# Kernel optimization log

Hardware: AMD Instinct MI355X
Metric: run time of the kernel (lower is better)

## Reference

```python
import jax, jax.numpy as jnp
import numpy as np

B, Q, E, NH, L, P = 8, 1024, 256, 8, 4, 4
DH = E // NH
SHAPES = np.array([[128, 128], [64, 64], [32, 32], [16, 16]], dtype=np.int64)
STARTS = np.concatenate([[0], np.cumsum(SHAPES.prod(1))[:-1]]).astype(np.int64)
S_TOTAL = int(SHAPES.prod(1).sum())
EPS = 1e-5


def setup_inputs() -> dict:
    key = jax.random.key(0)
    ks = iter(jax.random.split(key, 40))
    def rn(shp, s=0.02):
        return jax.random.normal(next(ks), shp, jnp.float32) * s
    return {
        "tgt": rn((B, Q, E), 1.0),
        "query_pos": rn((B, Q, E), 1.0),
        "reference_points": jax.random.uniform(next(ks), (B, Q, L, 2), jnp.float32),
        "src": rn((B, S_TOTAL, E), 1.0),
        "spatial_shapes": jnp.asarray(SHAPES),
        "level_start_index": jnp.asarray(STARTS),
        "in_proj_w": rn((3 * E, E)), "in_proj_b": jnp.zeros((3 * E,), jnp.float32),
        "out_proj_w": rn((E, E)), "out_proj_b": jnp.zeros((E,), jnp.float32),
        "norm1_g": jnp.ones((E,), jnp.float32), "norm1_b": jnp.zeros((E,), jnp.float32),
        "off_w": rn((NH * L * P * 2, E)), "off_b": rn((NH * L * P * 2,), 0.5),
        "aw_w": rn((NH * L * P, E)), "aw_b": jnp.zeros((NH * L * P,), jnp.float32),
        "vp_w": rn((E, E)), "vp_b": jnp.zeros((E,), jnp.float32),
        "op_w": rn((E, E)), "op_b": jnp.zeros((E,), jnp.float32),
        "norm2_g": jnp.ones((E,), jnp.float32), "norm2_b": jnp.zeros((E,), jnp.float32),
        "w1": rn((4 * E, E)), "b1": jnp.zeros((4 * E,), jnp.float32),
        "w2": rn((E, 4 * E)), "b2": jnp.zeros((E,), jnp.float32),
        "norm3_g": jnp.ones((E,), jnp.float32), "norm3_b": jnp.zeros((E,), jnp.float32),
    }


def _ln(x, g, b):
    mu = x.mean(-1, keepdims=True)
    var = ((x - mu) ** 2).mean(-1, keepdims=True)
    return (x - mu) * jax.lax.rsqrt(var + EPS) * g + b


def _bilinear(v, loc, Hl, Wl):
    # v: [B,NH,S_l,DH], loc in [0,1]: [B,NH,Q,P,2] -> [B,NH,Q,P,DH]
    # matches torch grid_sample(align_corners=False, padding='zeros')
    x = loc[..., 0] * Wl - 0.5
    y = loc[..., 1] * Hl - 0.5
    x0 = jnp.floor(x)
    y0 = jnp.floor(y)
    wx = (x - x0)[..., None]
    wy = (y - y0)[..., None]
    def g(yi, xi):
        valid = ((xi >= 0) & (xi <= Wl - 1) & (yi >= 0) & (yi <= Hl - 1)).astype(v.dtype)
        idx = (jnp.clip(yi, 0, Hl - 1) * Wl + jnp.clip(xi, 0, Wl - 1)).astype(jnp.int32)
        out = jnp.take_along_axis(v, idx.reshape(B, NH, Q * P, 1), axis=2)
        return out.reshape(B, NH, Q, P, DH) * valid[..., None]
    v00 = g(y0, x0); v01 = g(y0, x0 + 1.0)
    v10 = g(y0 + 1.0, x0); v11 = g(y0 + 1.0, x0 + 1.0)
    return (v00 * (1 - wy) * (1 - wx) + v01 * (1 - wy) * wx
            + v10 * wy * (1 - wx) + v11 * wy * wx)


def _forward(tgt, query_pos, reference_points, src,
             in_proj_w, in_proj_b, out_proj_w, out_proj_b, norm1_g, norm1_b,
             off_w, off_b, aw_w, aw_b, vp_w, vp_b, op_w, op_b,
             norm2_g, norm2_b, w1, b1, w2, b2, norm3_g, norm3_b,
             spatial_shapes, level_start_index):
    shp = np.asarray(spatial_shapes)
    starts = np.asarray(level_start_index)
    # ---- self-attention (q = k = tgt + pos, v = tgt) ----
    qk = tgt + query_pos
    wq, wk, wv = jnp.split(in_proj_w, 3, axis=0)
    bq, bk, bv = jnp.split(in_proj_b, 3, axis=0)
    q = (qk @ wq.T + bq).reshape(B, Q, NH, DH)
    k = (qk @ wk.T + bk).reshape(B, Q, NH, DH)
    v = (tgt @ wv.T + bv).reshape(B, Q, NH, DH)
    scores = jnp.einsum("bqhd,bkhd->bhqk", q, k) / jnp.sqrt(jnp.float32(DH))
    attn = jax.nn.softmax(scores, axis=-1)
    ctx = jnp.einsum("bhqk,bkhd->bqhd", attn, v).reshape(B, Q, E)
    tgt = _ln(tgt + (ctx @ out_proj_w.T + out_proj_b), norm1_g, norm1_b)
    # ---- MSDA cross-attention ----
    query = tgt + query_pos
    value = (src @ vp_w.T + vp_b).reshape(B, S_TOTAL, NH, DH).transpose(0, 2, 1, 3)  # [B,NH,S,DH]
    off = (query @ off_w.T + off_b).reshape(B, Q, NH, L, P, 2)
    aw = jax.nn.softmax((query @ aw_w.T + aw_b).reshape(B, Q, NH, L * P), -1)
    aw = aw.reshape(B, Q, NH, L, P)
    normalizer = jnp.asarray(shp[:, ::-1].copy(), jnp.float32)  # [L,2] = (W,H)
    loc = reference_points[:, :, None, :, None, :] + off / normalizer[None, None, None, :, None, :]
    loc = jnp.transpose(loc, (0, 2, 1, 3, 4, 5))  # [B,NH,Q,L,P,2]
    awt = jnp.transpose(aw, (0, 2, 1, 3, 4))      # [B,NH,Q,L,P]
    out = jnp.zeros((B, NH, Q, DH), jnp.float32)
    for l in range(L):
        Hl, Wl = int(shp[l, 0]), int(shp[l, 1])
        s0 = int(starts[l])
        vl = value[:, :, s0:s0 + Hl * Wl]
        samp = _bilinear(vl, loc[:, :, :, l], Hl, Wl)         # [B,NH,Q,P,DH]
        out = out + (samp * awt[:, :, :, l, :, None]).sum(3)
    ca = out.transpose(0, 2, 1, 3).reshape(B, Q, E) @ op_w.T + op_b
    tgt = _ln(tgt + ca, norm2_g, norm2_b)
    # ---- FFN ----
    h = jax.nn.relu(tgt @ w1.T + b1) @ w2.T + b2
    return _ln(tgt + h, norm3_g, norm3_b)


def reference(tgt, query_pos, reference_points, src, spatial_shapes, level_start_index,
              in_proj_w, in_proj_b, out_proj_w, out_proj_b, norm1_g, norm1_b,
              off_w, off_b, aw_w, aw_b, vp_w, vp_b, op_w, op_b,
              norm2_g, norm2_b, w1, b1, w2, b2, norm3_g, norm3_b):
    return _forward(tgt, query_pos, reference_points, src,
                    in_proj_w, in_proj_b, out_proj_w, out_proj_b, norm1_g, norm1_b,
                    off_w, off_b, aw_w, aw_b, vp_w, vp_b, op_w, op_b,
                    norm2_g, norm2_b, w1, b1, w2, b2, norm3_g, norm3_b,
                    spatial_shapes, level_start_index)
```

## Files before the change

### kernel.cpp

```cpp
#include <hip/hip_runtime.h>
#include <hip/hip_bf16.h>
#include <math.h>

typedef __hip_bfloat16 bf16;
typedef unsigned short ushort_t;

#define BQ 8
#define QLEN 1024
#define EMB 256
#define NHD 8
#define NLVL 4
#define NPT 4
#define DHD 32
#define STOT 21760

typedef short s8v __attribute__((ext_vector_type(8)));
typedef float f4v __attribute__((ext_vector_type(4)));

__device__ __forceinline__ float b2f(bf16 x) { return __bfloat162float(x); }

__device__ __forceinline__ float ldin(const void* p, int bf, size_t i) {
    return bf ? __bfloat162float(((const bf16*)p)[i]) : ((const float*)p)[i];
}

__device__ __forceinline__ float bfraw(unsigned u) {
    union { unsigned i; float f; } c; c.i = u << 16; return c.f;
}

__device__ __forceinline__ unsigned short f2us(float x) {
    bf16 h = __float2bfloat16(x);
    unsigned short u;
    __builtin_memcpy(&u, &h, 2);
    return u;
}

__global__ void detect_dtype(const unsigned* __restrict__ n1g, int* __restrict__ flag) {
    if (threadIdx.x == 0) flag[0] = (n1g[0] == 0x3F800000u) ? 0 : 1;
}

template <bool ARAW, bool RELU, typename CT, int WR, int WC>
__global__ __launch_bounds__(64 * WR * WC) void gemm_mfma(
        const void* __restrict__ A,
        const void* __restrict__ W, int w0,
        const void* __restrict__ bias, int b0,
        CT* __restrict__ C,
        int M, int N, int K,
        const int* __restrict__ dflag) {
    constexpr int T = 64 * WR * WC;
    constexpr int BM = 64 * WR, BN = 64 * WC;
    constexpr int AI = (BM * 4) / T;
    constexpr int BI = (BN * 4) / T;
    const int bfm = *dflag;
    __shared__ ushort_t As[BM][40];
    __shared__ ushort_t Bs[BN][40];
    const int tid = threadIdx.x;
    const int lane = tid & 63;
    const int wv = tid >> 6;
    const int wrow = (wv % WR) << 6;
    const int wcol = (wv / WR) << 6;
    const int m0 = blockIdx.x * BM, n0 = blockIdx.y * BN;
    const int l15 = lane & 15, lhi = lane >> 4;

    f4v acc[4][4] = {};

    uint4 ra[AI], rb[BI];
    float4 fa[AI][2], fb[BI][2];

    auto ld = [&](int k0) {
#pragma unroll
        for (int i = 0; i < AI; ++i) {
            const int idx = tid + T * i;
            const int r = idx >> 2, c = (idx & 3) << 3;
            const size_t aoff = (size_t)(m0 + r) * K + k0 + c;
            if (!ARAW || bfm) {
                ra[i] = *(const uint4*)((const ushort_t*)A + aoff);
            } else {
                const float* af = (const float*)A + aoff;
                fa[i][0] = *(const float4*)af;
                fa[i][1] = *(const float4*)(af + 4);
            }
        }
#pragma unroll
        for (int i = 0; i < BI; ++i) {
            const int idx = tid + T * i;
            const int r = idx >> 2, c = (idx & 3) << 3;
            const size_t woff = (size_t)(w0 + n0 + r) * K + k0 + c;
            if (bfm) {
                rb[i] = *(const uint4*)((const ushort_t*)W + woff);
            } else {
                const float* wf = (const float*)W + woff;
                fb[i][0] = *(const float4*)wf;
                fb[i][1] = *(const float4*)(wf + 4);
            }
        }
    };
    auto st = [&]() {
#pragma unroll
        for (int i = 0; i < AI; ++i) {
            const int idx = tid + T * i;
            const int r = idx >> 2, c = (idx & 3) << 3;
            if (!ARAW || bfm) {
                *(uint4*)&As[r][c] = ra[i];
            } else {
                ushort_t t[8] = {f2us(fa[i][0].x), f2us(fa[i][0].y), f2us(fa[i][0].z), f2us(fa[i][0].w),
                                 f2us(fa[i][1].x), f2us(fa[i][1].y), f2us(fa[i][1].z), f2us(fa[i][1].w)};
                *(uint4*)&As[r][c] = *(uint4*)t;
            }
        }
#pragma unroll
        for (int i = 0; i < BI; ++i) {
            const int idx = tid + T * i;
            const int r = idx >> 2, c = (idx & 3) << 3;
            if (bfm) {
                *(uint4*)&Bs[r][c] = rb[i];
            } else {
                ushort_t t[8] = {f2us(fb[i][0].x), f2us(fb[i][0].y), f2us(fb[i][0].z), f2us(fb[i][0].w),
                                 f2us(fb[i][1].x), f2us(fb[i][1].y), f2us(fb[i][1].z), f2us(fb[i][1].w)};
                *(uint4*)&Bs[r][c] = *(uint4*)t;
            }
        }
    };

    ld(0);
    for (int k0 = 0; k0 < K; k0 += 32) {
        st();
        __syncthreads();
        if (k0 + 32 < K) ld(k0 + 32);

        s8v afr[4], bfr[4];
#pragma unroll
        for (int i = 0; i < 4; ++i)
            afr[i] = *(const s8v*)&As[wrow + i * 16 + l15][lhi * 8];
#pragma unroll
        for (int j = 0; j < 4; ++j)
            bfr[j] = *(const s8v*)&Bs[wcol + j * 16 + l15][lhi * 8];
#pragma unroll
        for (int i = 0; i < 4; ++i)
#pragma unroll
            for (int j = 0; j < 4; ++j)
                acc[i][j] = __builtin_amdgcn_mfma_f32_16x16x32_bf16(
                    afr[i], bfr[j], acc[i][j], 0, 0, 0);
        __syncthreads();
    }

#pragma unroll
    for (int j = 0; j < 4; ++j) {
        const int n = n0 + wcol + j * 16 + l15;
        const float bv = ldin(bias, bfm, b0 + n);
#pragma unroll
        for (int i = 0; i < 4; ++i) {
#pragma unroll
            for (int p = 0; p < 4; ++p) {
                const int m = m0 + wrow + i * 16 + lhi * 4 + p;
                float v = acc[i][j][p] + bv;
                if (RELU) v = fmaxf(v, 0.f);
                if (sizeof(CT) == 2) ((ushort_t*)C)[(size_t)m * N + n] = f2us(v);
                else                 ((float*)C)[(size_t)m * N + n] = v;
            }
        }
    }
}

__global__ void ew_add_bf(const void* __restrict__ a, const void* __restrict__ b,
                          ushort_t* __restrict__ c, int n, const int* __restrict__ dflag) {
    const int bfm = *dflag;
    int i = blockIdx.x * 256 + threadIdx.x;
    if (i < n) c[i] = f2us(ldin(a, bfm, i) + ldin(b, bfm, i));
}

__global__ __launch_bounds__(256) void attn_mfma(const ushort_t* __restrict__ qkbuf,
                                                 const ushort_t* __restrict__ v,
                                                 ushort_t* __restrict__ ctx) {
    __shared__ ushort_t Ks[64][40];
    __shared__ ushort_t Vt[32][72];
    __shared__ ushort_t Ps[4][16][72];
    const int bh = blockIdx.y;
    const int b = bh >> 3, h = bh & 7;
    const int qt = blockIdx.x;
    const int tid = threadIdx.x;
    const int lane = tid & 63;
    const int wv = tid >> 6;
    const int l15 = lane & 15, quad = lane >> 4;
    const float scale = 0.17677669529663689f;

    const int qbase = (qt << 6) + (wv << 4);
    const s8v qfrag = *(const s8v*)(qkbuf +
        ((size_t)(b * QLEN + qbase + l15)) * 512 + h * DHD + quad * 8);

    const int sk = tid >> 2;
    const int sd = (tid & 3) << 3;

    float m_run[4] = {-1e30f, -1e30f, -1e30f, -1e30f};
    float l_run[4] = {};
    f4v o[2] = {};

    for (int kt = 0; kt < 16; ++kt) {
        __syncthreads();
        const size_t krow = (size_t)(b * QLEN + (kt << 6) + sk);
        *(uint4*)&Ks[sk][sd] = *(const uint4*)(qkbuf + krow * 512 + 256 + h * DHD + sd);
        const uint4 uv = *(const uint4*)(v + krow * 256 + h * DHD + sd);
        ushort_t vt[8];
        *(uint4*)vt = uv;
#pragma unroll
        for (int j = 0; j < 8; ++j) Vt[sd + j][sk] = vt[j];
        __syncthreads();

        f4v s4[4];
#pragma unroll
        for (int kb = 0; kb < 4; ++kb) {
            const s8v kfr = *(const s8v*)&Ks[(kb << 4) + l15][quad * 8];
            s4[kb] = __builtin_amdgcn_mfma_f32_16x16x32_bf16(qfrag, kfr, f4v{}, 0, 0, 0);
        }

        float sc[4][4];
#pragma unroll
        for (int kb = 0; kb < 4; ++kb)
#pragma unroll
            for (int p = 0; p < 4; ++p) sc[kb][p] = s4[kb][p] * scale;
        float mp[4];
#pragma unroll
        for (int p = 0; p < 4; ++p)
            mp[p] = fmaxf(fmaxf(sc[0][p], sc[1][p]), fmaxf(sc[2][p], sc[3][p]));
#pragma unroll
        for (int p = 0; p < 4; ++p) {
            mp[p] = fmaxf(mp[p], __shfl_xor(mp[p], 1, 64));
            mp[p] = fmaxf(mp[p], __shfl_xor(mp[p], 2, 64));
            mp[p] = fmaxf(mp[p], __shfl_xor(mp[p], 4, 64));
            mp[p] = fmaxf(mp[p], __shfl_xor(mp[p], 8, 64));
        }
        float al[4], ls[4] = {};
#pragma unroll
        for (int p = 0; p < 4; ++p) {
            const float mn = fmaxf(m_run[p], mp[p]);
            al[p] = __expf(m_run[p] - mn);
            m_run[p] = mn;
        }
        float pe[4][4];
#pragma unroll
        for (int kb = 0; kb < 4; ++kb)
#pragma unroll
            for (int p = 0; p < 4; ++p) {
                const float e = __expf(sc[kb][p] - m_run[p]);
                pe[kb][p] = e;
                ls[p] += e;
            }
#pragma unroll
        for (int p = 0; p < 4; ++p) {
            ls[p] += __shfl_xor(ls[p], 1, 64);
            ls[p] += __shfl_xor(ls[p], 2, 64);
            ls[p] += __shfl_xor(ls[p], 4, 64);
            ls[p] += __shfl_xor(ls[p], 8, 64);
            l_run[p] = l_run[p] * al[p] + ls[p];
        }
#pragma unroll
        for (int nb = 0; nb < 2; ++nb)
#pragma unroll
            for (int p = 0; p < 4; ++p) o[nb][p] *= al[p];

#pragma unroll
        for (int kb = 0; kb < 4; ++kb)
#pragma unroll
            for (int p = 0; p < 4; ++p)
                Ps[wv][(quad << 2) + p][(kb << 4) + l15] = f2us(pe[kb][p]);

#pragma unroll
        for (int kk = 0; kk < 2; ++kk) {
            const s8v afr = *(const s8v*)&Ps[wv][l15][kk * 32 + quad * 8];
#pragma unroll
            for (int nb = 0; nb < 2; ++nb) {
                const s8v bfr = *(const s8v*)&Vt[nb * 16 + l15][kk * 32 + quad * 8];
                o[nb] = __builtin_amdgcn_mfma_f32_16x16x32_bf16(afr, bfr, o[nb], 0, 0, 0);
            }
        }
    }

#pragma unroll
    for (int p = 0; p < 4; ++p) {
        const float inv = 1.f / l_run[p];
        const size_t row = (size_t)(b * QLEN + qbase + (quad << 2) + p) * EMB + h * DHD;
#pragma unroll
        for (int nb = 0; nb < 2; ++nb)
            ctx[row + nb * 16 + l15] = f2us(o[nb][p] * inv);
    }
}

__global__ __launch_bounds__(256) void ln_kernel(const void* __restrict__ xb,
                                                 const float* __restrict__ xf1,
                                                 const float* __restrict__ xf2,
                                                 const void* __restrict__ g,
                                                 const void* __restrict__ bta,
                                                 float* __restrict__ out_f,
                                                 ushort_t* __restrict__ out_b,
                                                 void* __restrict__ out_d,
                                                 const void* __restrict__ qp,
                                                 ushort_t* __restrict__ out_q,
                                                 const int* __restrict__ dflag) {
    const int bf = *dflag;
    const int row = blockIdx.x, t = threadIdx.x;
    const size_t base = (size_t)row * EMB + t;
    float x = 0.f;
    if (xb) x += ldin(xb, bf, base);
    if (xf1) x += xf1[base];
    if (xf2) x += xf2[base];
    __shared__ float red[256];
    red[t] = x;
    __syncthreads();
    for (int o = 128; o > 0; o >>= 1) { if (t < o) red[t] += red[t + o]; __syncthreads(); }
    const float mu = red[0] * (1.f / EMB);
    __syncthreads();
    const float dx = x - mu;
    red[t] = dx * dx;
    __syncthreads();
    for (int o = 128; o > 0; o >>= 1) { if (t < o) red[t] += red[t + o]; __syncthreads(); }
    const float var = red[0] * (1.f / EMB);
    const float y = dx * rsqrtf(var + 1e-5f) * ldin(g, bf, t) + ldin(bta, bf, t);
    if (out_f) out_f[base] = y;
    if (out_b) out_b[base] = f2us(y);
    if (out_d) {
        if (bf) ((ushort_t*)out_d)[base] = f2us(y);
        else    ((float*)out_d)[base] = y;
    }
    if (out_q) out_q[base] = f2us(y + ldin(qp, bf, base));
}

__global__ __launch_bounds__(64) void sample_kernel(const float* __restrict__ offb,
                                                    const float* __restrict__ awb,
                                                    const void* __restrict__ refp,
                                                    const ushort_t* __restrict__ value,
                                                    ushort_t* __restrict__ out,
                                                    const int* __restrict__ dflag) {
    const int bf = *dflag;
    const int bid = blockIdx.x;
    const int h = bid & 7;
    const int bq = bid >> 3;
    const int b = bq >> 10;
    const int lane = threadIdx.x;
    const int s_idx = lane >> 2;
    const int dg = lane & 3;
    const int l = s_idx >> 2;

    float logit = awb[(size_t)bq * 128 + h * 16 + s_idx];
    float m = logit;
#pragma unroll
    for (int o = 32; o > 0; o >>= 1) m = fmaxf(m, __shfl_xor(m, o, 64));
    float e = __expf(logit - m);
    float ssum = e;
#pragma unroll
    for (int o = 32; o > 0; o >>= 1) ssum += __shfl_xor(ssum, o, 64);
    const float paw = 4.f * e / ssum;

    const int Wi = 128 >> l;
    const float Wl = (float)Wi, Hl = (float)Wi;
    const int s0 = (l == 0) ? 0 : (l == 1) ? 16384 : (l == 2) ? 20480 : 21504;

    const float rx = ldin(refp, bf, ((size_t)bq * NLVL + l) * 2 + 0);
    const float ry = ldin(refp, bf, ((size_t)bq * NLVL + l) * 2 + 1);
    const float ox = offb[(size_t)bq * 256 + h * 32 + s_idx * 2 + 0];
    const float oy = offb[(size_t)bq * 256 + h * 32 + s_idx * 2 + 1];
    const float x = (rx + ox / Wl) * Wl - 0.5f;
    const float y = (ry + oy / Hl) * Hl - 0.5f;
    const float x0 = floorf(x), y0 = floorf(y);
    const float wx = x - x0, wy = y - y0;

    float acc[8] = {};
    const ushort_t* vbase = value + ((size_t)b * STOT) * EMB + h * DHD + dg * 8;

    auto corner = [&](float yi, float xi, float w) {
        const bool valid = (xi >= 0.f) && (xi <= Wl - 1.f) && (yi >= 0.f) && (yi <= Hl - 1.f);
        const float xc = fminf(fmaxf(xi, 0.f), Wl - 1.f);
        const float yc = fminf(fmaxf(yi, 0.f), Hl - 1.f);
        const int row = s0 + (int)yc * Wi + (int)xc;
        const uint4 u = *(const uint4*)(vbase + (size_t)row * EMB);
        const float wv = valid ? w : 0.f;
        const unsigned ua[4] = {u.x, u.y, u.z, u.w};
#pragma unroll
        for (int j = 0; j < 4; ++j) {
            acc[2 * j + 0] = fmaf(wv, bfraw(ua[j] & 0xffffu), acc[2 * j + 0]);
            acc[2 * j + 1] = fmaf(wv, bfraw(ua[j] >> 16), acc[2 * j + 1]);
        }
    };
    corner(y0, x0, (1.f - wy) * (1.f - wx));
    corner(y0, x0 + 1.f, (1.f - wy) * wx);
    corner(y0 + 1.f, x0, wy * (1.f - wx));
    corner(y0 + 1.f, x0 + 1.f, wy * wx);

#pragma unroll
    for (int j = 0; j < 8; ++j) {
        float vj = acc[j] * paw;
        vj += __shfl_xor(vj, 4, 64);
        vj += __shfl_xor(vj, 8, 64);
        vj += __shfl_xor(vj, 16, 64);
        vj += __shfl_xor(vj, 32, 64);
        acc[j] = vj;
    }
    if (s_idx == 0) {
        ushort_t t[8];
#pragma unroll
        for (int j = 0; j < 8; ++j) t[j] = f2us(acc[j]);
        *(uint4*)(out + (size_t)bq * EMB + h * DHD + dg * 8) = *(uint4*)t;
    }
}

extern "C" void kernel_launch(void* const* d_in, const int* in_sizes, int n_in,
                              void* d_out, int out_size, void* d_ws, size_t ws_size,
                              hipStream_t stream) {
    const void* tgt  = d_in[0];
    const void* qp   = d_in[1];
    const void* refp = d_in[2];
    const void* src  = d_in[3];
    const void* ipw  = d_in[6];
    const void* ipb  = d_in[7];
    const void* oprw = d_in[8];
    const void* oprb = d_in[9];
    const void* n1g  = d_in[10];
    const void* n1b  = d_in[11];
    const void* ofw  = d_in[12];
    const void* ofb  = d_in[13];
    const void* aww  = d_in[14];
    const void* awbv = d_in[15];
    const void* vpw  = d_in[16];
    const void* vpb  = d_in[17];
    const void* opw2 = d_in[18];
    const void* opb2 = d_in[19];
    const void* n2g  = d_in[20];
    const void* n2b  = d_in[21];
    const void* w1   = d_in[22];
    const void* b1   = d_in[23];
    const void* w2   = d_in[24];
    const void* b2   = d_in[25];
    const void* n3g  = d_in[26];
    const void* n3b  = d_in[27];

    const int M = BQ * QLEN;
    const int MS = BQ * STOT;

    char* ws = (char*)d_ws;
    int* dflag = (int*)ws;
    size_t o = 256;
    char* S1 = ws + o; o += (size_t)M * EMB * 2;
    char* S2 = ws + o; o += (size_t)M * 512 * 2;
    char* S3 = ws + o; o += (size_t)M * EMB * 2;
    char* S4 = ws + o; o += (size_t)M * EMB * 2;
    char* S5 = ws + o; o += (size_t)M * EMB * 4;
    char* S6 = ws + o; o += (size_t)M * EMB * 4;
    char* S7 = ws + o; o += (size_t)M * EMB * 4;
    char* S8 = ws + o;

    ushort_t* qk_bf    = (ushort_t*)S1;
    ushort_t* samp_bf  = (ushort_t*)S1;
    ushort_t* qkproj   = (ushort_t*)S2;
    float*    off_f    = (float*)S2;
    ushort_t* vproj    = (ushort_t*)S3;
    ushort_t* qry_bf   = (ushort_t*)S3;
    ushort_t* tgt2_bf  = (ushort_t*)S3;
    ushort_t* ctx_bf   = (ushort_t*)S4;
    float*    awl_f    = (float*)S4;
    float*    bufD     = (float*)S5;
    float*    tgt1_f   = (float*)S6;
    float*    tgt2_f   = (float*)S7;
    ushort_t* value_bf = (ushort_t*)S8;
    ushort_t* h1_bf    = (ushort_t*)S8;

    detect_dtype<<<1, 64, 0, stream>>>((const unsigned*)n1g, dflag);

    ew_add_bf<<<(M * EMB) / 256, 256, 0, stream>>>(tgt, qp, qk_bf, M * EMB, dflag);
    gemm_mfma<false, false, ushort_t, 1, 2><<<dim3(M / 64, 4), 128, 0, stream>>>(
        qk_bf, ipw, 0, ipb, 0, qkproj, M, 512, 256, dflag);
    gemm_mfma<true, false, ushort_t, 1, 2><<<dim3(M / 64, 2), 128, 0, stream>>>(
        tgt, ipw, 512, ipb, 512, vproj, M, 256, 256, dflag);
    attn_mfma<<<dim3(16, BQ * NHD), 256, 0, stream>>>(qkproj, vproj, ctx_bf);
    gemm_mfma<false, false, float, 1, 2><<<dim3(M / 64, 2), 128, 0, stream>>>(
        ctx_bf, oprw, 0, oprb, 0, bufD, M, 256, 256, dflag);
    ln_kernel<<<M, 256, 0, stream>>>(tgt, bufD, nullptr, n1g, n1b,
                                     tgt1_f, nullptr, nullptr, qp, qry_bf, dflag);

    gemm_mfma<false, false, float, 1, 2><<<dim3(M / 64, 2), 128, 0, stream>>>(
        qry_bf, ofw, 0, ofb, 0, off_f, M, 256, 256, dflag);
    gemm_mfma<false, false, float, 1, 2><<<dim3(M / 64, 1), 128, 0, stream>>>(
        qry_bf, aww, 0, awbv, 0, awl_f, M, 128, 256, dflag);
    gemm_mfma<true, false, ushort_t, 2, 4><<<dim3(MS / 128, 1), 512, 0, stream>>>(
        src, vpw, 0, vpb, 0, value_bf, MS, 256, 256, dflag);
    sample_kernel<<<M * NHD, 64, 0, stream>>>(off_f, awl_f, refp, value_bf, samp_bf, dflag);
    gemm_mfma<false, false, float, 1, 2><<<dim3(M / 64, 2), 128, 0, stream>>>(
        samp_bf, opw2, 0, opb2, 0, bufD, M, 256, 256, dflag);
    ln_kernel<<<M, 256, 0, stream>>>(nullptr, tgt1_f, bufD, n2g, n2b,
                                     tgt2_f, tgt2_bf, nullptr, nullptr, nullptr, dflag);

    gemm_mfma<false, true, ushort_t, 1, 2><<<dim3(M / 64, 8), 128, 0, stream>>>(
        tgt2_bf, w1, 0, b1, 0, h1_bf, M, 1024, 256, dflag);
    gemm_mfma<false, false, float, 1, 2><<<dim3(M / 64, 2), 128, 0, stream>>>(
        h1_bf, w2, 0, b2, 0, bufD, M, 256, 1024, dflag);
    ln_kernel<<<M, 256, 0, stream>>>(nullptr, tgt2_f, bufD, n3g, n3b,
                                     nullptr, nullptr, d_out, nullptr, nullptr, dflag);
}
```

Measured before the change: 687.0 us.

## Use direct global-to-LDS loads with XOR swizzle and LDS-staged coalesced GEMM epilogue

The GEMM now stages A/W tiles into LDS with global_load_lds (16-byte direct loads), replacing the register-staged loads. Unpadded LDS rows get an XOR swizzle to avoid bank conflicts. The epilogue goes through per-wave LDS scratch so each lane writes a 16-byte vector instead of scattered 2- or 4-byte stores. The register prefetch of the next K tile is dropped, so global loads no longer overlap with MFMA within a block. The fp32 path also loses its earlier latency hiding.

```diff
diff --git a/kernel.cpp b/kernel.cpp
--- a/kernel.cpp
+++ b/kernel.cpp
@@ -32,6 +32,12 @@
     unsigned short u;
     __builtin_memcpy(&u, &h, 2);
     return u;
+}
+
+typedef const __attribute__((address_space(1))) unsigned int* gas1_u32;
+typedef __attribute__((address_space(3))) unsigned int* las3_u32;
+__device__ __forceinline__ void gload_lds16(const void* g, void* l) {
+    __builtin_amdgcn_global_load_lds((gas1_u32)g, (las3_u32)l, 16, 0, 0);
 }
 
 __global__ void detect_dtype(const unsigned* __restrict__ n1g, int* __restrict__ flag) {
@@ -47,12 +53,19 @@
         int M, int N, int K,
         const int* __restrict__ dflag) {
     constexpr int T = 64 * WR * WC;
+    constexpr int NW = WR * WC;
     constexpr int BM = 64 * WR, BN = 64 * WC;
-    constexpr int AI = (BM * 4) / T;
-    constexpr int BI = (BN * 4) / T;
+    constexpr int ACH = (BM * 4) / T;
+    constexpr int BCH = (BN * 4) / T;
+    constexpr int STAGE_US = (BM + BN) * 32;
+    constexpr int EPI_US = NW * 16 * 88;
+    constexpr int SMEM_US = STAGE_US > EPI_US ? STAGE_US : EPI_US;
+
     const int bfm = *dflag;
-    __shared__ ushort_t As[BM][40];
-    __shared__ ushort_t Bs[BN][40];
+    __shared__ __align__(16) ushort_t smem[SMEM_US];
+    ushort_t* As = smem;
+    ushort_t* Bs = smem + BM * 32;
+
     const int tid = threadIdx.x;
     const int lane = tid & 63;
     const int wv = tid >> 6;
@@ -60,80 +73,60 @@
     const int wcol = (wv / WR) << 6;
     const int m0 = blockIdx.x * BM, n0 = blockIdx.y * BN;
     const int l15 = lane & 15, lhi = lane >> 4;
+    const int swz = (l15 >> 1) & 3;
 
     f4v acc[4][4] = {};
 
-    uint4 ra[AI], rb[BI];
-    float4 fa[AI][2], fb[BI][2];
-
-    auto ld = [&](int k0) {
-#pragma unroll
-        for (int i = 0; i < AI; ++i) {
-            const int idx = tid + T * i;
-            const int r = idx >> 2, c = (idx & 3) << 3;
-            const size_t aoff = (size_t)(m0 + r) * K + k0 + c;
+    auto stage = [&](int k0) {
+#pragma unroll
+        for (int i = 0; i < ACH; ++i) {
+            const int s0 = (wv << 6) + T * i;
+            const int s = s0 + lane;
+            const int r = s >> 2;
+            const int gd = (s & 3) ^ ((r >> 1) & 3);
+            const size_t aoff = (size_t)(m0 + r) * K + k0 + gd * 8;
             if (!ARAW || bfm) {
-                ra[i] = *(const uint4*)((const ushort_t*)A + aoff);
+                gload_lds16((const ushort_t*)A + aoff, As + (size_t)s0 * 8);
             } else {
                 const float* af = (const float*)A + aoff;
-                fa[i][0] = *(const float4*)af;
-                fa[i][1] = *(const float4*)(af + 4);
-            }
-        }
-#pragma unroll
-        for (int i = 0; i < BI; ++i) {
-            const int idx = tid + T * i;
-            const int r = idx >> 2, c = (idx & 3) << 3;
-            const size_t woff = (size_t)(w0 + n0 + r) * K + k0 + c;
+                const float4 f0 = *(const float4*)af;
+                const float4 f1 = *(const float4*)(af + 4);
+                ushort_t t[8] = {f2us(f0.x), f2us(f0.y), f2us(f0.z), f2us(f0.w),
+                                 f2us(f1.x), f2us(f1.y), f2us(f1.z), f2us(f1.w)};
+                *(uint4*)(As + (size_t)s * 8) = *(uint4*)t;
+            }
+        }
+#pragma unroll
+        for (int i = 0; i < BCH; ++i) {
+            const int s0 = (wv << 6) + T * i;
+            const int s = s0 + lane;
+            const int r = s >> 2;
+            const int gd = (s & 3) ^ ((r >> 1) & 3);
+            const size_t woff = (size_t)(w0 + n0 + r) * K + k0 + gd * 8;
             if (bfm) {
-                rb[i] = *(const uint4*)((const ushort_t*)W + woff);
+                gload_lds16((const ushort_t*)W + woff, Bs + (size_t)s0 * 8);
             } else {
                 const float* wf = (const float*)W + woff;
-                fb[i][0] = *(const float4*)wf;
-                fb[i][1] = *(const float4*)(wf + 4);
+                const float4 f0 = *(const float4*)wf;
+                const float4 f1 = *(const float4*)(wf + 4);
+                ushort_t t[8] = {f2us(f0.x), f2us(f0.y), f2us(f0.z), f2us(f0.w),
+                                 f2us(f1.x), f2us(f1.y), f2us(f1.z), f2us(f1.w)};
+                *(uint4*)(Bs + (size_t)s * 8) = *(uint4*)t;
             }
         }
     };
-    auto st = [&]() {
-#pragma unroll
-        for (int i = 0; i < AI; ++i) {
-            const int idx = tid + T * i;
-            const int r = idx >> 2, c = (idx & 3) << 3;
-            if (!ARAW || bfm) {
-                *(uint4*)&As[r][c] = ra[i];
-            } else {
-                ushort_t t[8] = {f2us(fa[i][0].x), f2us(fa[i][0].y), f2us(fa[i][0].z), f2us(fa[i][0].w),
-                                 f2us(fa[i][1].x), f2us(fa[i][1].y), f2us(fa[i][1].z), f2us(fa[i][1].w)};
-                *(uint4*)&As[r][c] = *(uint4*)t;
-            }
-        }
-#pragma unroll
-        for (int i = 0; i < BI; ++i) {
-            const int idx = tid + T * i;
-            const int r = idx >> 2, c = (idx & 3) << 3;
-            if (bfm) {
-                *(uint4*)&Bs[r][c] = rb[i];
-            } else {
-                ushort_t t[8] = {f2us(fb[i][0].x), f2us(fb[i][0].y), f2us(fb[i][0].z), f2us(fb[i][0].w),
-                                 f2us(fb[i][1].x), f2us(fb[i][1].y), f2us(fb[i][1].z), f2us(fb[i][1].w)};
-                *(uint4*)&Bs[r][c] = *(uint4*)t;
-            }
-        }
-    };
-
-    ld(0);
+
     for (int k0 = 0; k0 < K; k0 += 32) {
-        st();
+        stage(k0);
         __syncthreads();
-        if (k0 + 32 < K) ld(k0 + 32);
 
         s8v afr[4], bfr[4];
 #pragma unroll
         for (int i = 0; i < 4; ++i)
-            afr[i] = *(const s8v*)&As[wrow + i * 16 + l15][lhi * 8];
+            afr[i] = *(const s8v*)(As + (wrow + i * 16 + l15) * 32 + ((lhi ^ swz) << 3));
 #pragma unroll
         for (int j = 0; j < 4; ++j)
-            bfr[j] = *(const s8v*)&Bs[wcol + j * 16 + l15][lhi * 8];
+            bfr[j] = *(const s8v*)(Bs + (wcol + j * 16 + l15) * 32 + ((lhi ^ swz) << 3));
 #pragma unroll
         for (int i = 0; i < 4; ++i)
 #pragma unroll
@@ -143,19 +136,58 @@
         __syncthreads();
     }
 
-#pragma unroll
-    for (int j = 0; j < 4; ++j) {
-        const int n = n0 + wcol + j * 16 + l15;
-        const float bv = ldin(bias, bfm, b0 + n);
+    if (sizeof(CT) == 2) {
+        ushort_t* eb = smem + wv * 16 * 88;
 #pragma unroll
         for (int i = 0; i < 4; ++i) {
 #pragma unroll
-            for (int p = 0; p < 4; ++p) {
-                const int m = m0 + wrow + i * 16 + lhi * 4 + p;
-                float v = acc[i][j][p] + bv;
-                if (RELU) v = fmaxf(v, 0.f);
-                if (sizeof(CT) == 2) ((ushort_t*)C)[(size_t)m * N + n] = f2us(v);
-                else                 ((float*)C)[(size_t)m * N + n] = v;
+            for (int j = 0; j < 4; ++j) {
+                const int n = n0 + wcol + j * 16 + l15;
+                const float bv = ldin(bias, bfm, b0 + n);
+#pragma unroll
+                for (int p = 0; p < 4; ++p) {
+                    float v = acc[i][j][p] + bv;
+                    if (RELU) v = fmaxf(v, 0.f);
+                    eb[(lhi * 4 + p) * 88 + j * 16 + l15] = f2us(v);
+                }
+            }
+#pragma unroll
+            for (int pass = 0; pass < 2; ++pass) {
+                const int row = pass * 8 + (lane >> 3);
+                const int g = lane & 7;
+                const uint4 u = *(const uint4*)(eb + row * 88 + g * 8);
+                const int m = m0 + wrow + i * 16 + row;
+                const int n = n0 + wcol + g * 8;
+                *(uint4*)((ushort_t*)C + (size_t)m * N + n) = u;
+            }
+        }
+    } else {
+        float* ef = (float*)smem + wv * 16 * 44;
+#pragma unroll
+        for (int i = 0; i < 4; ++i) {
+#pragma unroll
+            for (int jp = 0; jp < 2; ++jp) {
+#pragma unroll
+                for (int j2 = 0; j2 < 2; ++j2) {
+                    const int j = jp * 2 + j2;
+                    const int n = n0 + wcol + j * 16 + l15;
+                    const float bv = ldin(bias, bfm, b0 + n);
+#pragma unroll
+                    for (int p = 0; p < 4; ++p) {
+                        float v = acc[i][j][p] + bv;
+                        if (RELU) v = fmaxf(v, 0.f);
+                        ef[(lhi * 4 + p) * 44 + j2 * 16 + l15] = v;
+                    }
+                }
+#pragma unroll
+                for (int pass = 0; pass < 2; ++pass) {
+                    const int row = pass * 8 + (lane >> 3);
+                    const int g = lane & 7;
+                    const float4 u = *(const float4*)(ef + row * 44 + g * 4);
+                    const int m = m0 + wrow + i * 16 + row;
+                    const int n = n0 + wcol + jp * 32 + g * 4;
+                    *(float4*)((float*)C + (size_t)m * N + n) = u;
+                }
             }
         }
     }
```

Result: slower. 738.3 us (+7.5%).
